# Optimization experiments

Hardware: AMD Instinct MI355X
Metric: run time of the kernel (lower is better)

The kernel has to match this reference:

```python
import jax, jax.numpy as jnp
import numpy as np

R = 0.5  # init kwarg r; reduction='mean'
N = 8192


def setup_inputs() -> dict:
    key = jax.random.key(0)
    k1, k2, k3 = jax.random.split(key, 3)
    pred = jax.random.normal(k1, (N, 1), dtype=jnp.float32)
    time = jax.random.uniform(k2, (N,), dtype=jnp.float32) * 100.0  # survival times
    event = jax.random.randint(k3, (N,), 0, 2).astype(jnp.float32)  # censoring indicator in {0,1}
    target = jnp.stack([time, event], axis=1)  # [N, 2]
    return {"pred": pred, "target": target}


def reference(pred, target):
    p = pred.squeeze(-1)            # [n]
    time = target[:, 0]             # [n]
    event = target[:, 1]            # [n]

    diff = p - time
    diff = jnp.where(event == 0, jnp.maximum(diff, 0.0), diff)
    regression_loss = jnp.mean(diff * diff)

    # ranking branch over all n^2 ordered pairs (i=index2 slow, j=index1 fast):
    # valid pair iff time[j] > time[i] and event[i] == 1
    mask = (time[None, :] > time[:, None]) & (event[:, None] == 1)  # [n, n] bool
    hinge = jnp.maximum(1.0 - p[None, :] + p[:, None], 0.0)         # [n, n]
    cnt = jnp.maximum(mask.sum(), 1).astype(jnp.float32)            # dynamic pair count -> masked mean
    ranking_loss = jnp.sum(jnp.where(mask, hinge * hinge, 0.0)) / cnt

    return R * ranking_loss + (1.0 - R) * regression_loss
```

## Files before the change

### kernel.cpp

```cpp
#include <hip/hip_runtime.h>

#define BLK 256
#define ITILE 256
#define GX 32
#define GY 32
#define NSLOTS (GX * GY)

__global__ __launch_bounds__(BLK) void svm_partial(
    const float* __restrict__ pred,
    const float2* __restrict__ tg,
    float* __restrict__ ws_rank,
    float* __restrict__ ws_reg,
    unsigned int* __restrict__ ws_cnt) {
  const int tid = threadIdx.x;
  const int i0 = blockIdx.x * ITILE;
  const int j0 = blockIdx.y * BLK;

  const float pj = pred[j0 + tid];
  const float tj = tg[j0 + tid].x;

  float rank = 0.0f;
  unsigned long long cnt = 0ull;

  for (int ib = 0; ib < ITILE; ib += 8) {
    float pi[8], ti[8], ei[8];
    #pragma unroll
    for (int u = 0; u < 8; ++u) {
      pi[u] = pred[i0 + ib + u];
      float2 te = tg[i0 + ib + u];
      ti[u] = te.x;
      ei[u] = te.y;
    }
    #pragma unroll
    for (int u = 0; u < 8; ++u) {
      if (ei[u] == 1.0f) {
        const float pi1 = pi[u] + 1.0f;
        const bool m = tj > ti[u];
        cnt += __popcll(__ballot(m));
        float h = m ? (pi1 - pj) : 0.0f;
        h = fmaxf(h, 0.0f);
        rank = fmaf(h, h, rank);
      }
    }
  }

  float reg = 0.0f;
  if (blockIdx.y == 0) {
    const int i = i0 + tid;
    const float p = pred[i];
    const float2 te = tg[i];
    float d = p - te.x;
    if (te.y == 0.0f) d = fmaxf(d, 0.0f);
    reg = d * d;
  }

  #pragma unroll
  for (int off = 32; off > 0; off >>= 1) {
    rank += __shfl_down(rank, off);
    reg  += __shfl_down(reg, off);
  }

  __shared__ float sr[BLK / 64];
  __shared__ float sg[BLK / 64];
  __shared__ unsigned long long sc[BLK / 64];
  const int wave = tid >> 6;
  const int lane = tid & 63;
  if (lane == 0) { sr[wave] = rank; sg[wave] = reg; sc[wave] = cnt; }
  __syncthreads();

  if (tid == 0) {
    float r = 0.f, g = 0.f;
    unsigned long long c = 0ull;
    #pragma unroll
    for (int w = 0; w < BLK / 64; ++w) { r += sr[w]; g += sg[w]; c += sc[w]; }
    const int slot = blockIdx.y * GX + blockIdx.x;
    ws_rank[slot] = r;
    ws_reg[slot]  = g;
    ws_cnt[slot]  = (unsigned int)c;
  }
}

__global__ __launch_bounds__(BLK) void svm_finalize(
    const float* __restrict__ ws_rank,
    const float* __restrict__ ws_reg,
    const unsigned int* __restrict__ ws_cnt,
    float* __restrict__ out, int n) {
  const int tid = threadIdx.x;
  double r = 0.0, g = 0.0;
  unsigned long long c = 0ull;
  for (int s = tid; s < NSLOTS; s += BLK) {
    r += (double)ws_rank[s];
    g += (double)ws_reg[s];
    c += (unsigned long long)ws_cnt[s];
  }
  #pragma unroll
  for (int off = 32; off > 0; off >>= 1) {
    r += __shfl_down(r, off);
    g += __shfl_down(g, off);
    c += __shfl_down(c, off);
  }
  __shared__ double dr[BLK / 64];
  __shared__ double dg[BLK / 64];
  __shared__ unsigned long long dc[BLK / 64];
  const int wave = tid >> 6;
  const int lane = tid & 63;
  if (lane == 0) { dr[wave] = r; dg[wave] = g; dc[wave] = c; }
  __syncthreads();
  if (tid == 0) {
    r = dr[0] + dr[1] + dr[2] + dr[3];
    g = dg[0] + dg[1] + dg[2] + dg[3];
    c = dc[0] + dc[1] + dc[2] + dc[3];
    const double cd = (double)(c > 0ull ? c : 1ull);
    out[0] = (float)(0.5 * r / cd + 0.5 * g / (double)n);
  }
}

extern "C" void kernel_launch(void* const* d_in, const int* in_sizes, int n_in,
                              void* d_out, int out_size, void* d_ws, size_t ws_size,
                              hipStream_t stream) {
  const float* pred = (const float*)d_in[0];
  const float2* tg = (const float2*)d_in[1];
  float* out = (float*)d_out;
  const int n = in_sizes[0];

  float* ws_rank = (float*)d_ws;
  float* ws_reg  = (float*)((char*)d_ws + NSLOTS * sizeof(float));
  unsigned int* ws_cnt = (unsigned int*)((char*)d_ws + 2 * NSLOTS * sizeof(float));

  dim3 grid(GX, GY);
  svm_partial<<<grid, BLK, 0, stream>>>(pred, tg, ws_rank, ws_reg, ws_cnt);
  svm_finalize<<<1, BLK, 0, stream>>>(ws_rank, ws_reg, ws_cnt, out, n);
}
```

Baseline: 72.81 us.

## Fuse partial and finalize kernels via last-block atomic reduction, retile grid

Replaces the two-kernel scheme (partials to workspace plus a single-block finalize) with one kernel. Each block atomically adds its partial sums to device globals, and the last block to arrive computes the output and resets the counters. It also halves the i-tile to 128 rows, doubling the grid to 2048 blocks, and widens the inner unroll to 16. The aim is to remove a launch and the tail serialization, and to improve occupancy across CUs. In exchange, float atomic accumulation becomes order-nondeterministic, and global atomics contend on a few addresses.

```diff
diff --git a/kernel.cpp b/kernel.cpp
--- a/kernel.cpp
+++ b/kernel.cpp
@@ -1,17 +1,21 @@
 #include <hip/hip_runtime.h>
 
 #define BLK 256
-#define ITILE 256
-#define GX 32
+#define ITILE 128
+#define IB 16
+#define GX 64
 #define GY 32
-#define NSLOTS (GX * GY)
+#define NBLOCKS (GX * GY)
+#define NPAD 32
 
-__global__ __launch_bounds__(BLK) void svm_partial(
+__device__ float g_sums[2 * NPAD];
+__device__ unsigned int g_u[2 * NPAD];
+
+__global__ __launch_bounds__(BLK) void svm_fused(
     const float* __restrict__ pred,
     const float2* __restrict__ tg,
-    float* __restrict__ ws_rank,
-    float* __restrict__ ws_reg,
-    unsigned int* __restrict__ ws_cnt) {
+    float* __restrict__ out,
+    int n) {
   const int tid = threadIdx.x;
   const int i0 = blockIdx.x * ITILE;
   const int j0 = blockIdx.y * BLK;
@@ -20,23 +24,23 @@
   const float tj = tg[j0 + tid].x;
 
   float rank = 0.0f;
-  unsigned long long cnt = 0ull;
+  unsigned int cnt = 0u;
 
-  for (int ib = 0; ib < ITILE; ib += 8) {
-    float pi[8], ti[8], ei[8];
+  for (int ib = 0; ib < ITILE; ib += IB) {
+    float pi[IB], ti[IB], ei[IB];
     #pragma unroll
-    for (int u = 0; u < 8; ++u) {
+    for (int u = 0; u < IB; ++u) {
       pi[u] = pred[i0 + ib + u];
       float2 te = tg[i0 + ib + u];
       ti[u] = te.x;
       ei[u] = te.y;
     }
     #pragma unroll
-    for (int u = 0; u < 8; ++u) {
+    for (int u = 0; u < IB; ++u) {
       if (ei[u] == 1.0f) {
         const float pi1 = pi[u] + 1.0f;
         const bool m = tj > ti[u];
-        cnt += __popcll(__ballot(m));
+        cnt += (unsigned int)__popcll(__ballot(m));
         float h = m ? (pi1 - pj) : 0.0f;
         h = fmaxf(h, 0.0f);
         rank = fmaf(h, h, rank);
@@ -45,7 +49,7 @@
   }
 
   float reg = 0.0f;
-  if (blockIdx.y == 0) {
+  if (blockIdx.y == 0 && tid < ITILE) {
     const int i = i0 + tid;
     const float p = pred[i];
     const float2 te = tg[i];
@@ -62,56 +66,35 @@
 
   __shared__ float sr[BLK / 64];
   __shared__ float sg[BLK / 64];
-  __shared__ unsigned long long sc[BLK / 64];
+  __shared__ unsigned int sc[BLK / 64];
   const int wave = tid >> 6;
   const int lane = tid & 63;
   if (lane == 0) { sr[wave] = rank; sg[wave] = reg; sc[wave] = cnt; }
   __syncthreads();
 
   if (tid == 0) {
-    float r = 0.f, g = 0.f;
-    unsigned long long c = 0ull;
-    #pragma unroll
-    for (int w = 0; w < BLK / 64; ++w) { r += sr[w]; g += sg[w]; c += sc[w]; }
-    const int slot = blockIdx.y * GX + blockIdx.x;
-    ws_rank[slot] = r;
-    ws_reg[slot]  = g;
-    ws_cnt[slot]  = (unsigned int)c;
-  }
-}
+    const float r = sr[0] + sr[1] + sr[2] + sr[3];
+    const float g = sg[0] + sg[1] + sg[2] + sg[3];
+    const unsigned int c = sc[0] + sc[1] + sc[2] + sc[3];
 
-__global__ __launch_bounds__(BLK) void svm_finalize(
-    const float* __restrict__ ws_rank,
-    const float* __restrict__ ws_reg,
-    const unsigned int* __restrict__ ws_cnt,
-    float* __restrict__ out, int n) {
-  const int tid = threadIdx.x;
-  double r = 0.0, g = 0.0;
-  unsigned long long c = 0ull;
-  for (int s = tid; s < NSLOTS; s += BLK) {
-    r += (double)ws_rank[s];
-    g += (double)ws_reg[s];
-    c += (unsigned long long)ws_cnt[s];
-  }
-  #pragma unroll
-  for (int off = 32; off > 0; off >>= 1) {
-    r += __shfl_down(r, off);
-    g += __shfl_down(g, off);
-    c += __shfl_down(c, off);
-  }
-  __shared__ double dr[BLK / 64];
-  __shared__ double dg[BLK / 64];
-  __shared__ unsigned long long dc[BLK / 64];
-  const int wave = tid >> 6;
-  const int lane = tid & 63;
-  if (lane == 0) { dr[wave] = r; dg[wave] = g; dc[wave] = c; }
-  __syncthreads();
-  if (tid == 0) {
-    r = dr[0] + dr[1] + dr[2] + dr[3];
-    g = dg[0] + dg[1] + dg[2] + dg[3];
-    c = dc[0] + dc[1] + dc[2] + dc[3];
-    const double cd = (double)(c > 0ull ? c : 1ull);
-    out[0] = (float)(0.5 * r / cd + 0.5 * g / (double)n);
+    atomicAdd(&g_sums[0], r);
+    atomicAdd(&g_sums[NPAD], g);
+    atomicAdd(&g_u[0], c);
+    __threadfence();
+    const unsigned int t = atomicAdd(&g_u[NPAD], 1u);
+    if (t == NBLOCKS - 1u) {
+      __threadfence();
+      const float rr = atomicAdd(&g_sums[0], 0.0f);
+      const float gg = atomicAdd(&g_sums[NPAD], 0.0f);
+      const unsigned int cc = atomicAdd(&g_u[0], 0u);
+      const double cd = (double)(cc > 0u ? cc : 1u);
+      out[0] = (float)(0.5 * (double)rr / cd + 0.5 * (double)gg / (double)n);
+      atomicExch(&g_sums[0], 0.0f);
+      atomicExch(&g_sums[NPAD], 0.0f);
+      atomicExch(&g_u[0], 0u);
+      __threadfence();
+      atomicExch(&g_u[NPAD], 0u);
+    }
   }
 }
 
@@ -121,13 +104,7 @@
   const float* pred = (const float*)d_in[0];
   const float2* tg = (const float2*)d_in[1];
   float* out = (float*)d_out;
-  const int n = in_sizes[0];
+  int n = in_sizes[0];
 
-  float* ws_rank = (float*)d_ws;
-  float* ws_reg  = (float*)((char*)d_ws + NSLOTS * sizeof(float));
-  unsigned int* ws_cnt = (unsigned int*)((char*)d_ws + 2 * NSLOTS * sizeof(float));
-
-  dim3 grid(GX, GY);
-  svm_partial<<<grid, BLK, 0, stream>>>(pred, tg, ws_rank, ws_reg, ws_cnt);
-  svm_finalize<<<1, BLK, 0, stream>>>(ws_rank, ws_reg, ws_cnt, out, n);
+  svm_fused<<<dim3(GX, GY), BLK, 0, stream>>>(pred, tg, out, n);
 }
```

Result: slower. 104.5 us (+43.6%).
